# Performance work log

Hardware: AMD Instinct MI355X
Metric: run time of the kernel (lower is better)

Reference implementation:

```python
import jax, jax.numpy as jnp
import numpy as np

H = W = 56; WS = 7; SHIFT = 3; NH = 6; DIM = 192; DEPTH = 2
HD = DIM // NH; NW = (H // WS) * (W // WS); N = WS * WS; SCALE = HD ** -0.5

# relative position index (constant, as in WindowAttention.__init__)
_c = np.stack(np.meshgrid(np.arange(WS), np.arange(WS), indexing='ij')).reshape(2, -1)
_r = (_c[:, :, None] - _c[:, None, :]).transpose(1, 2, 0)
_r[..., 0] += WS - 1; _r[..., 1] += WS - 1; _r[..., 0] *= 2 * WS - 1
RPI = jnp.asarray(_r.sum(-1).reshape(-1))  # (N*N,)

def _build_mask():
    # shifted-window attention mask (constant, built in SwinTransformerBlock.__init__)
    img = np.zeros((H, W))
    sl = (slice(0, -WS), slice(-WS, -SHIFT), slice(-SHIFT, None))
    cnt = 0
    for hs in sl:
        for ws_ in sl:
            img[hs, ws_] = cnt; cnt += 1
    mw = img.reshape(H // WS, WS, W // WS, WS).transpose(0, 2, 1, 3).reshape(-1, N)
    am = mw[:, None, :] - mw[:, :, None]  # (nW, N, N)
    return jnp.asarray(np.where(am != 0, -100.0, 0.0).astype(np.float32))

MASK = _build_mask()

def _ln(x, g, b):
    m = jnp.mean(x, -1, keepdims=True)
    v = jnp.mean((x - m) ** 2, -1, keepdims=True)
    return (x - m) * jax.lax.rsqrt(v + 1e-5) * g + b

def setup_inputs() -> dict:
    key = jax.random.key(0)
    ks = jax.random.split(key, 8)
    B = 64; s = 0.02
    return {
        'x': jax.random.normal(ks[0], (B, H * W, DIM), jnp.float32),
        'norm1_g': jnp.ones((DEPTH, DIM), jnp.float32),
        'norm1_b': jnp.zeros((DEPTH, DIM), jnp.float32),
        'qkv_w': jax.random.normal(ks[1], (DEPTH, DIM, 3 * DIM), jnp.float32) * s,
        'qkv_b': jnp.zeros((DEPTH, 3 * DIM), jnp.float32),
        'rpb': jax.random.normal(ks[2], (DEPTH, (2 * WS - 1) ** 2, NH), jnp.float32) * s,
        'proj_w': jax.random.normal(ks[3], (DEPTH, DIM, DIM), jnp.float32) * s,
        'proj_b': jnp.zeros((DEPTH, DIM), jnp.float32),
        'norm2_g': jnp.ones((DEPTH, DIM), jnp.float32),
        'norm2_b': jnp.zeros((DEPTH, DIM), jnp.float32),
        'fc1_w': jax.random.normal(ks[4], (DEPTH, DIM, 4 * DIM), jnp.float32) * s,
        'fc1_b': jnp.zeros((DEPTH, 4 * DIM), jnp.float32),
        'fc2_w': jax.random.normal(ks[5], (DEPTH, 4 * DIM, DIM), jnp.float32) * s,
        'fc2_b': jnp.zeros((DEPTH, DIM), jnp.float32),
    }

def reference(x, norm1_g, norm1_b, qkv_w, qkv_b, rpb, proj_w, proj_b,
              norm2_g, norm2_b, fc1_w, fc1_b, fc2_w, fc2_b):
    B = x.shape[0]
    for i in range(DEPTH):
        shift = 0 if i % 2 == 0 else WS // 2
        # --- windowed MHSA branch ---
        h = _ln(x, norm1_g[i], norm1_b[i]).reshape(B, H, W, DIM)
        if shift:
            h = jnp.roll(h, (-shift, -shift), (1, 2))
        # window partition -> (B*nW, N, C)
        w = h.reshape(B, H // WS, WS, W // WS, WS, DIM)
        w = w.transpose(0, 1, 3, 2, 4, 5).reshape(B * NW, N, DIM)
        qkv = (w @ qkv_w[i] + qkv_b[i]).reshape(B * NW, N, 3, NH, HD)
        qkv = qkv.transpose(2, 0, 3, 1, 4)  # (3, Bw, NH, N, HD)
        q, k, v = qkv[0] * SCALE, qkv[1], qkv[2]
        attn = jnp.einsum('bhnd,bhmd->bhnm', q, k)  # (Bw, NH, N, N)
        bias = rpb[i][RPI].reshape(N, N, NH).transpose(2, 0, 1)
        attn = attn + bias[None]
        if shift:
            attn = attn.reshape(B, NW, NH, N, N) + MASK[None, :, None]
            attn = attn.reshape(B * NW, NH, N, N)
        attn = jax.nn.softmax(attn, axis=-1)
        o = jnp.einsum('bhnm,bhmd->bhnd', attn, v)
        o = o.transpose(0, 2, 1, 3).reshape(B * NW, N, DIM)
        o = o @ proj_w[i] + proj_b[i]
        # window reverse
        h = o.reshape(B, H // WS, W // WS, WS, WS, DIM)
        h = h.transpose(0, 1, 3, 2, 4, 5).reshape(B, H, W, DIM)
        if shift:
            h = jnp.roll(h, (shift, shift), (1, 2))
        x = x + h.reshape(B, H * W, DIM)
        # --- MLP branch ---
        m = _ln(x, norm2_g[i], norm2_b[i])
        m = jax.nn.gelu(m @ fc1_w[i] + fc1_b[i], approximate=False)
        x = x + (m @ fc2_w[i] + fc2_b[i])
    return x
```

## Files before the change

### kernel.cpp

```cpp
#include <hip/hip_runtime.h>
#include <stdint.h>

#define MROWS  200704
#define SCALE_ 0.17677669529663687f

typedef __attribute__((ext_vector_type(8))) short bf16x8;
typedef __attribute__((ext_vector_type(4))) float f32x4;
union V8 { uint4 u; unsigned short s[8]; };

__device__ __forceinline__ float bf2f(unsigned short u) {
  union { unsigned int i; float f; } c; c.i = ((unsigned int)u) << 16; return c.f;
}
__device__ __forceinline__ unsigned short f2bf(float f) {
  union { float f; unsigned int i; } c; c.f = f;
  unsigned int lsb = (c.i >> 16) & 1;
  return (unsigned short)((c.i + 0x7fffu + lsb) >> 16);
}

typedef __attribute__((address_space(1))) const void gas_t;
typedef __attribute__((address_space(3))) void las_t;
__device__ __forceinline__ void gload16(const void* g, void* l) {
  __builtin_amdgcn_global_load_lds((gas_t*)g, (las_t*)l, 16, 0, 0);
}

__device__ __forceinline__ bf16x8 ard(const unsigned short* As, int row, int k) {
  return *reinterpret_cast<const bf16x8*>(As + row * 192 + (((k >> 3) ^ (row & 7)) << 3));
}
__device__ __forceinline__ void awr(unsigned short* As, int row, int c, unsigned short v) {
  As[row * 192 + (((c >> 3) ^ (row & 7)) << 3) + (c & 7)] = v;
}
template<int RS>
__device__ __forceinline__ void stage_a(const unsigned short* __restrict__ src,
                                        unsigned short* As, int wv, int lane, int colofs) {
  #pragma unroll
  for (int i = 0; i < 12; ++i) {
    int g = wv * 768 + i * 64 + lane;
    int row = g / 24, c = g - row * 24;
    int sc = c ^ (row & 7);
    gload16(src + (size_t)row * RS + colofs + sc * 8, As + (wv * 768 + i * 64) * 8);
  }
}
__device__ __forceinline__ void ln_row(const float* __restrict__ xr,
    const float* __restrict__ g, const float* __restrict__ b,
    unsigned short* As, int row, int lane) {
  float v0 = xr[lane], v1 = xr[lane + 64], v2 = xr[lane + 128];
  float s  = v0 + v1 + v2;
  float s2 = v0*v0 + v1*v1 + v2*v2;
  #pragma unroll
  for (int m = 32; m >= 1; m >>= 1) { s += __shfl_xor(s, m); s2 += __shfl_xor(s2, m); }
  float mean = s * (1.0f/192.0f);
  float var  = s2 * (1.0f/192.0f) - mean*mean;
  float inv  = rsqrtf(var + 1e-5f);
  awr(As, row, lane,       f2bf((v0-mean)*inv*g[lane]      + b[lane]));
  awr(As, row, lane+64,    f2bf((v1-mean)*inv*g[lane+64]   + b[lane+64]));
  awr(As, row, lane+128,   f2bf((v2-mean)*inv*g[lane+128]  + b[lane+128]));
}
__device__ __forceinline__ void panel_mm(const bf16x8 (&afr)[6][4],
    const unsigned short* __restrict__ Wp, int kq, f32x4 (&acc)[4][2]) {
  bf16x8 bfr[6][2];
  #pragma unroll
  for (int ks = 0; ks < 6; ++ks) {
    bfr[ks][0] = *reinterpret_cast<const bf16x8*>(Wp + ks*32 + kq);
    bfr[ks][1] = *reinterpret_cast<const bf16x8*>(Wp + 16*192 + ks*32 + kq);
  }
  #pragma unroll
  for (int ks = 0; ks < 6; ++ks)
    #pragma unroll
    for (int mi = 0; mi < 4; ++mi) {
      acc[mi][0] = __builtin_amdgcn_mfma_f32_16x16x32_bf16(afr[ks][mi], bfr[ks][0], acc[mi][0], 0, 0, 0);
      acc[mi][1] = __builtin_amdgcn_mfma_f32_16x16x32_bf16(afr[ks][mi], bfr[ks][1], acc[mi][1], 0, 0, 0);
    }
}

__global__ __launch_bounds__(256) void wt_k(const float* __restrict__ W,
    unsigned short* __restrict__ Wt, int K, int N)
{
  int idx = blockIdx.x * 256 + threadIdx.x;
  if (idx < K * N) {
    int k = idx / N, n = idx - k * N;
    Wt[(size_t)n * K + k] = f2bf(W[idx]);
  }
}

__global__ __launch_bounds__(256, 2) void qkv_k(const float* __restrict__ X,
    const float* __restrict__ g, const float* __restrict__ b,
    const unsigned short* __restrict__ Wt, const float* __restrict__ bias,
    unsigned short* __restrict__ C, int shift)
{
  __shared__ unsigned short As[128 * 192];
  const int tid = threadIdx.x, lane = tid & 63, wv = tid >> 6;
  const int row0 = blockIdx.x * 128;
  #pragma unroll 2
  for (int r = 0; r < 32; ++r) {
    int row = wv * 32 + r, wr = row0 + row;
    int win = wr / 49, n = wr - win * 49;
    int bi = win >> 6, w64 = win & 63, wh = w64 >> 3, ww = w64 & 7;
    int ti = n / 7, tj = n - ti * 7;
    int gh = wh*7 + ti + shift; if (gh >= 56) gh -= 56;
    int gw = ww*7 + tj + shift; if (gw >= 56) gw -= 56;
    ln_row(X + ((size_t)bi*3136 + gh*56 + gw)*192, g, b, As, row, lane);
  }
  __syncthreads();
  const int wm = wv >> 1, wn = wv & 1, fr = lane & 15, kq = (lane >> 4) * 8;
  bf16x8 afr[6][4];
  #pragma unroll
  for (int ks = 0; ks < 6; ++ks)
    #pragma unroll
    for (int mi = 0; mi < 4; ++mi)
      afr[ks][mi] = ard(As, wm*64 + mi*16 + fr, ks*32 + kq);
  const int lcol = lane & 15, lr4 = (lane >> 4) * 4;
  #pragma unroll 2
  for (int p = 0; p < 9; ++p) {
    f32x4 acc[4][2] = {};
    panel_mm(afr, Wt + (size_t)(p*64 + wn*32 + fr) * 192, kq, acc);
    #pragma unroll
    for (int mi = 0; mi < 4; ++mi)
    #pragma unroll
    for (int ni = 0; ni < 2; ++ni)
    #pragma unroll
    for (int i = 0; i < 4; ++i) {
      int gr = row0 + wm*64 + mi*16 + lr4 + i;
      int gc = p*64 + wn*32 + ni*16 + lcol;
      C[(size_t)gr * 576 + gc] = f2bf(acc[mi][ni][i] + bias[gc]);
    }
  }
}

__global__ __launch_bounds__(256, 2) void proj_k(const unsigned short* __restrict__ A,
    const unsigned short* __restrict__ Wt, const float* __restrict__ bias,
    const float* __restrict__ Xres, float* __restrict__ Xdst, int shift)
{
  __shared__ unsigned short As[128 * 192];
  const int tid = threadIdx.x, lane = tid & 63, wv = tid >> 6;
  const int row0 = blockIdx.x * 128;
  stage_a<192>(A + (size_t)row0 * 192, As, wv, lane, 0);
  __syncthreads();
  const int wm = wv >> 1, wn = wv & 1, fr = lane & 15, kq = (lane >> 4) * 8;
  bf16x8 afr[6][4];
  #pragma unroll
  for (int ks = 0; ks < 6; ++ks)
    #pragma unroll
    for (int mi = 0; mi < 4; ++mi)
      afr[ks][mi] = ard(As, wm*64 + mi*16 + fr, ks*32 + kq);
  const int lcol = lane & 15, lr4 = (lane >> 4) * 4;
  int rbase[16];
  #pragma unroll
  for (int mi = 0; mi < 4; ++mi)
  #pragma unroll
  for (int i = 0; i < 4; ++i) {
    int gr = row0 + wm*64 + mi*16 + lr4 + i;
    int win = gr / 49, n = gr - win * 49;
    int bi = win >> 6, w64 = win & 63, wh = w64 >> 3, ww = w64 & 7;
    int ti = n / 7, tj = n - ti * 7;
    int gh = wh*7 + ti + shift; if (gh >= 56) gh -= 56;
    int gw = ww*7 + tj + shift; if (gw >= 56) gw -= 56;
    rbase[mi*4 + i] = (bi*3136 + gh*56 + gw) * 192;
  }
  #pragma unroll
  for (int p = 0; p < 3; ++p) {
    f32x4 acc[4][2] = {};
    panel_mm(afr, Wt + (size_t)(p*64 + wn*32 + fr) * 192, kq, acc);
    #pragma unroll
    for (int mi = 0; mi < 4; ++mi)
    #pragma unroll
    for (int ni = 0; ni < 2; ++ni)
    #pragma unroll
    for (int i = 0; i < 4; ++i) {
      int gc = p*64 + wn*32 + ni*16 + lcol;
      size_t idx = (size_t)rbase[mi*4 + i] + gc;
      Xdst[idx] = Xres[idx] + acc[mi][ni][i] + bias[gc];
    }
  }
}

__global__ __launch_bounds__(256, 2) void fc1_k(const float* __restrict__ X,
    const float* __restrict__ g, const float* __restrict__ b,
    const unsigned short* __restrict__ Wt, const float* __restrict__ bias,
    unsigned short* __restrict__ H)
{
  __shared__ unsigned short As[128 * 192];
  const int tid = threadIdx.x, lane = tid & 63, wv = tid >> 6;
  const int row0 = blockIdx.x * 128;
  #pragma unroll 2
  for (int r = 0; r < 32; ++r) {
    int row = wv * 32 + r;
    ln_row(X + (size_t)(row0 + row) * 192, g, b, As, row, lane);
  }
  __syncthreads();
  const int wm = wv >> 1, wn = wv & 1, fr = lane & 15, kq = (lane >> 4) * 8;
  bf16x8 afr[6][4];
  #pragma unroll
  for (int ks = 0; ks < 6; ++ks)
    #pragma unroll
    for (int mi = 0; mi < 4; ++mi)
      afr[ks][mi] = ard(As, wm*64 + mi*16 + fr, ks*32 + kq);
  const int lcol = lane & 15, lr4 = (lane >> 4) * 4;
  #pragma unroll 2
  for (int p = 0; p < 12; ++p) {
    f32x4 acc[4][2] = {};
    panel_mm(afr, Wt + (size_t)(p*64 + wn*32 + fr) * 192, kq, acc);
    #pragma unroll
    for (int mi = 0; mi < 4; ++mi)
    #pragma unroll
    for (int ni = 0; ni < 2; ++ni)
    #pragma unroll
    for (int i = 0; i < 4; ++i) {
      int gr = row0 + wm*64 + mi*16 + lr4 + i;
      int gc = p*64 + wn*32 + ni*16 + lcol;
      float v = acc[mi][ni][i] + bias[gc];
      float gv = 0.5f * v * (1.0f + erff(v * 0.70710678118654752f));
      H[(size_t)gr * 768 + gc] = f2bf(gv);
    }
  }
}

__global__ __launch_bounds__(256, 2) void fc2_k(const unsigned short* __restrict__ H,
    const unsigned short* __restrict__ Wt,
    const float* __restrict__ bias, const float* __restrict__ Xres,
    float* __restrict__ Y)
{
  __shared__ unsigned short As[128 * 192];
  const int tid = threadIdx.x, lane = tid & 63, wv = tid >> 6;
  const int row0 = blockIdx.x * 128;
  const int wm = wv >> 1, wn = wv & 1, fr = lane & 15, kq = (lane >> 4) * 8;
  f32x4 acc[3][4][2] = {};
  for (int q = 0; q < 4; ++q) {
    if (q) __syncthreads();
    stage_a<768>(H + (size_t)row0 * 768, As, wv, lane, q * 192);
    __syncthreads();
    #pragma unroll
    for (int ks = 0; ks < 6; ++ks) {
      bf16x8 afr[4];
      #pragma unroll
      for (int mi = 0; mi < 4; ++mi)
        afr[mi] = ard(As, wm*64 + mi*16 + fr, ks*32 + kq);
      #pragma unroll
      for (int p = 0; p < 3; ++p) {
        const unsigned short* wp = Wt + (size_t)(p*64 + wn*32 + fr) * 768 + q*192 + ks*32 + kq;
        bf16x8 b0 = *reinterpret_cast<const bf16x8*>(wp);
        bf16x8 b1 = *reinterpret_cast<const bf16x8*>(wp + 16*768);
        #pragma unroll
        for (int mi = 0; mi < 4; ++mi) {
          acc[p][mi][0] = __builtin_amdgcn_mfma_f32_16x16x32_bf16(afr[mi], b0, acc[p][mi][0], 0, 0, 0);
          acc[p][mi][1] = __builtin_amdgcn_mfma_f32_16x16x32_bf16(afr[mi], b1, acc[p][mi][1], 0, 0, 0);
        }
      }
    }
  }
  const int lcol = lane & 15, lr4 = (lane >> 4) * 4;
  #pragma unroll
  for (int p = 0; p < 3; ++p)
  #pragma unroll
  for (int mi = 0; mi < 4; ++mi)
  #pragma unroll
  for (int ni = 0; ni < 2; ++ni)
  #pragma unroll
  for (int i = 0; i < 4; ++i) {
    int grow = row0 + wm*64 + mi*16 + lr4 + i;
    int gc = p*64 + wn*32 + ni*16 + lcol;
    float v = acc[p][mi][ni][i] + bias[gc];
    size_t idx = (size_t)grow * 192 + gc;
    Y[idx] = Xres[idx] + v;
  }
}

template<bool SHIFTED>
__global__ __launch_bounds__(64) void attn_k(
    const unsigned short* __restrict__ qkv,
    const float* __restrict__ rpb,
    unsigned short* __restrict__ out)
{
  __shared__ float kv[2][49][32];
  int blk = blockIdx.x;
  int win = blk / 6, h = blk - win * 6;
  int lane = threadIdx.x;
  const unsigned short* base = qkv + (size_t)win * 49 * 576;
  for (int idx = lane; idx < 196; idx += 64) {
    int n = idx >> 2, sg = (idx & 3) * 8;
    V8 kk, vv;
    kk.u = *reinterpret_cast<const uint4*>(base + n*576 + 192 + h*32 + sg);
    vv.u = *reinterpret_cast<const uint4*>(base + n*576 + 384 + h*32 + sg);
    #pragma unroll
    for (int j = 0; j < 8; ++j) { kv[0][n][sg+j] = bf2f(kk.s[j]); kv[1][n][sg+j] = bf2f(vv.s[j]); }
  }
  __syncthreads();
  if (lane < 49) {
    float q[32];
    const unsigned short* qr = base + (size_t)lane * 576 + h * 32;
    #pragma unroll
    for (int sg = 0; sg < 4; ++sg) {
      V8 qq; qq.u = *reinterpret_cast<const uint4*>(qr + sg*8);
      #pragma unroll
      for (int j = 0; j < 8; ++j) q[sg*8+j] = bf2f(qq.s[j]) * SCALE_;
    }
    int ti = lane / 7, tj = lane - ti * 7;
    int wi = win & 63, wh = wi >> 3, ww = wi & 7;
    int rid = 0;
    if (SHIFTED) {
      int hh = wh*7 + ti, wg = ww*7 + tj;
      rid = (hh < 49 ? 0 : (hh < 53 ? 1 : 2)) * 3 + (wg < 49 ? 0 : (wg < 53 ? 1 : 2));
    }
    float s[49];
    float mx = -1e30f;
    #pragma unroll
    for (int m = 0; m < 49; ++m) {
      float a = 0.f;
      #pragma unroll
      for (int d4 = 0; d4 < 8; ++d4) {
        float4 kf = *reinterpret_cast<const float4*>(&kv[0][m][d4*4]);
        a += q[d4*4+0]*kf.x + q[d4*4+1]*kf.y + q[d4*4+2]*kf.z + q[d4*4+3]*kf.w;
      }
      int mi = m / 7, mj = m - mi * 7;
      a += rpb[((ti - mi + 6) * 13 + (tj - mj + 6)) * 6 + h];
      if (SHIFTED) {
        int hh = wh*7 + mi, wg = ww*7 + mj;
        int rid2 = (hh < 49 ? 0 : (hh < 53 ? 1 : 2)) * 3 + (wg < 49 ? 0 : (wg < 53 ? 1 : 2));
        if (rid2 != rid) a -= 100.f;
      }
      s[m] = a;
      mx = fmaxf(mx, a);
    }
    float sum = 0.f;
    #pragma unroll
    for (int m = 0; m < 49; ++m) { float e = __expf(s[m] - mx); s[m] = e; sum += e; }
    float rs = 1.f / sum;
    float o[32];
    #pragma unroll
    for (int d = 0; d < 32; ++d) o[d] = 0.f;
    #pragma unroll
    for (int m = 0; m < 49; ++m) {
      float p = s[m] * rs;
      #pragma unroll
      for (int d4 = 0; d4 < 8; ++d4) {
        float4 vf = *reinterpret_cast<const float4*>(&kv[1][m][d4*4]);
        o[d4*4+0] += p*vf.x; o[d4*4+1] += p*vf.y; o[d4*4+2] += p*vf.z; o[d4*4+3] += p*vf.w;
      }
    }
    unsigned short* orow = out + ((size_t)win * 49 + lane) * 192 + h * 32;
    #pragma unroll
    for (int sg = 0; sg < 4; ++sg) {
      V8 pk;
      #pragma unroll
      for (int j = 0; j < 8; ++j) pk.s[j] = f2bf(o[sg*8+j]);
      *reinterpret_cast<uint4*>(orow + sg*8) = pk.u;
    }
  }
}

extern "C" void kernel_launch(void* const* d_in, const int* in_sizes, int n_in,
                              void* d_out, int out_size, void* d_ws, size_t ws_size,
                              hipStream_t stream) {
  const float* x    = (const float*)d_in[0];
  const float* n1g  = (const float*)d_in[1];
  const float* n1b  = (const float*)d_in[2];
  const float* qkvw = (const float*)d_in[3];
  const float* qkvb = (const float*)d_in[4];
  const float* rpb  = (const float*)d_in[5];
  const float* pw   = (const float*)d_in[6];
  const float* pb   = (const float*)d_in[7];
  const float* n2g  = (const float*)d_in[8];
  const float* n2b  = (const float*)d_in[9];
  const float* f1w  = (const float*)d_in[10];
  const float* f1b  = (const float*)d_in[11];
  const float* f2w  = (const float*)d_in[12];
  const float* f2b  = (const float*)d_in[13];
  float* out = (float*)d_out;

  const size_t XBYTES = (size_t)MROWS * 192 * 4;
  const size_t QBYTES = (size_t)MROWS * 576 * 2;
  const size_t ABYTES = (size_t)MROWS * 192 * 2;
  char* ws = (char*)d_ws;
  float* x1 = (float*)ws;
  unsigned short* Bbuf = (unsigned short*)(ws + XBYTES);
  unsigned short* Abuf = (unsigned short*)(ws + XBYTES + QBYTES);
  unsigned short* Hbuf = Bbuf;
  unsigned short* WT   = (unsigned short*)(ws + XBYTES + QBYTES + ABYTES);
  const size_t WQ = 110592, WP = 36864, W1 = 147456, W2 = 147456;
  const size_t WD = WQ + WP + W1 + W2;

  for (int d = 0; d < 2; ++d) {
    unsigned short* wt = WT + d * WD;
    wt_k<<<(int)((WQ + 255)/256), 256, 0, stream>>>(qkvw + (size_t)d*WQ, wt,                 192, 576);
    wt_k<<<(int)((WP + 255)/256), 256, 0, stream>>>(pw   + (size_t)d*WP, wt + WQ,            192, 192);
    wt_k<<<(int)((W1 + 255)/256), 256, 0, stream>>>(f1w  + (size_t)d*W1, wt + WQ + WP,       192, 768);
    wt_k<<<(int)((W2 + 255)/256), 256, 0, stream>>>(f2w  + (size_t)d*W2, wt + WQ + WP + W1,  768, 192);
  }

  const int GB = MROWS / 128;

  for (int i = 0; i < 2; ++i) {
    int shift = i ? 3 : 0;
    const float* xin = i ? (const float*)x1 : x;
    float* xfin = i ? out : x1;
    const unsigned short* wt = WT + i * WD;
    qkv_k<<<GB, 256, 0, stream>>>(xin, n1g + i*192, n1b + i*192, wt, qkvb + i*576, Bbuf, shift);
    if (shift) attn_k<true ><<<4096*6, 64, 0, stream>>>(Bbuf, rpb + i*169*6, Abuf);
    else       attn_k<false><<<4096*6, 64, 0, stream>>>(Bbuf, rpb + i*169*6, Abuf);
    proj_k<<<GB, 256, 0, stream>>>(Abuf, wt + WQ, pb + i*192, xin, x1, shift);
    fc1_k<<<GB, 256, 0, stream>>>(x1, n2g + i*192, n2b + i*192, wt + WQ + WP, f1b + i*768, Hbuf);
    fc2_k<<<GB, 256, 0, stream>>>(Hbuf, wt + WQ + WP + W1, f2b + i*192, x1, xfin);
  }
}
```

Measured before the change: 2.072 ms.

## Fuse fc1+GELU+fc2 into one MLP kernel and vectorize GEMM epilogues

Replaces the separate fc1 and fc2 kernels with a single mlp_k that keeps the 64x768 hidden activation chunked in shared memory, so the bf16 hidden tensor never goes to global memory. Exact erf GELU is replaced by a tanh-form approximation computed with exp and rcp. The qkv and proj MFMAs swap operand order so each lane holds four consecutive columns, which allows packed bf16 and float4 epilogue stores. Risks are GELU approximation error, lower MFMA reuse per block with 64-row tiles, and W1/W2 being re-read from global per block.

Result: slower. 2.309 ms (+11.4%).

```diff
diff --git a/kernel.cpp b/kernel.cpp
--- a/kernel.cpp
+++ b/kernel.cpp
@@ -15,6 +15,19 @@
   union { float f; unsigned int i; } c; c.f = f;
   unsigned int lsb = (c.i >> 16) & 1;
   return (unsigned short)((c.i + 0x7fffu + lsb) >> 16);
+}
+__device__ __forceinline__ uint2 pack4(float a, float b, float c, float d) {
+  uint2 r;
+  r.x = (unsigned)f2bf(a) | ((unsigned)f2bf(b) << 16);
+  r.y = (unsigned)f2bf(c) | ((unsigned)f2bf(d) << 16);
+  return r;
+}
+__device__ __forceinline__ float gelu_f(float x) {
+  float x2 = x * x;
+  float arg = x * fmaf(0.07135481f, x2, 1.59576912f);
+  float e = __expf(arg);
+  float r = __builtin_amdgcn_rcpf(1.0f + e);
+  return fmaf(-x, r, x);
 }
 
 typedef __attribute__((address_space(1))) const void gas_t;
@@ -55,7 +68,7 @@
   awr(As, row, lane+64,    f2bf((v1-mean)*inv*g[lane+64]   + b[lane+64]));
   awr(As, row, lane+128,   f2bf((v2-mean)*inv*g[lane+128]  + b[lane+128]));
 }
-__device__ __forceinline__ void panel_mm(const bf16x8 (&afr)[6][4],
+__device__ __forceinline__ void panel_mmS(const bf16x8 (&afr)[6][4],
     const unsigned short* __restrict__ Wp, int kq, f32x4 (&acc)[4][2]) {
   bf16x8 bfr[6][2];
   #pragma unroll
@@ -67,8 +80,8 @@
   for (int ks = 0; ks < 6; ++ks)
     #pragma unroll
     for (int mi = 0; mi < 4; ++mi) {
-      acc[mi][0] = __builtin_amdgcn_mfma_f32_16x16x32_bf16(afr[ks][mi], bfr[ks][0], acc[mi][0], 0, 0, 0);
-      acc[mi][1] = __builtin_amdgcn_mfma_f32_16x16x32_bf16(afr[ks][mi], bfr[ks][1], acc[mi][1], 0, 0, 0);
+      acc[mi][0] = __builtin_amdgcn_mfma_f32_16x16x32_bf16(bfr[ks][0], afr[ks][mi], acc[mi][0], 0, 0, 0);
+      acc[mi][1] = __builtin_amdgcn_mfma_f32_16x16x32_bf16(bfr[ks][1], afr[ks][mi], acc[mi][1], 0, 0, 0);
     }
 }
 
@@ -101,27 +114,27 @@
     ln_row(X + ((size_t)bi*3136 + gh*56 + gw)*192, g, b, As, row, lane);
   }
   __syncthreads();
-  const int wm = wv >> 1, wn = wv & 1, fr = lane & 15, kq = (lane >> 4) * 8;
+  const int wm = wv >> 1, wn = wv & 1, l15 = lane & 15, kq = (lane >> 4) * 8, qd = lane >> 4;
   bf16x8 afr[6][4];
   #pragma unroll
   for (int ks = 0; ks < 6; ++ks)
     #pragma unroll
     for (int mi = 0; mi < 4; ++mi)
-      afr[ks][mi] = ard(As, wm*64 + mi*16 + fr, ks*32 + kq);
-  const int lcol = lane & 15, lr4 = (lane >> 4) * 4;
+      afr[ks][mi] = ard(As, wm*64 + mi*16 + l15, ks*32 + kq);
   #pragma unroll 2
   for (int p = 0; p < 9; ++p) {
     f32x4 acc[4][2] = {};
-    panel_mm(afr, Wt + (size_t)(p*64 + wn*32 + fr) * 192, kq, acc);
+    panel_mmS(afr, Wt + (size_t)(p*64 + wn*32 + l15) * 192, kq, acc);
     #pragma unroll
     for (int mi = 0; mi < 4; ++mi)
     #pragma unroll
-    for (int ni = 0; ni < 2; ++ni)
-    #pragma unroll
-    for (int i = 0; i < 4; ++i) {
-      int gr = row0 + wm*64 + mi*16 + lr4 + i;
-      int gc = p*64 + wn*32 + ni*16 + lcol;
-      C[(size_t)gr * 576 + gc] = f2bf(acc[mi][ni][i] + bias[gc]);
+    for (int ni = 0; ni < 2; ++ni) {
+      int row = row0 + wm*64 + mi*16 + l15;
+      int col = p*64 + wn*32 + ni*16 + qd*4;
+      float4 bv = *reinterpret_cast<const float4*>(bias + col);
+      uint2 pk = pack4(acc[mi][ni][0]+bv.x, acc[mi][ni][1]+bv.y,
+                       acc[mi][ni][2]+bv.z, acc[mi][ni][3]+bv.w);
+      *reinterpret_cast<uint2*>(C + (size_t)row * 576 + col) = pk;
     }
   }
 }
@@ -135,132 +148,139 @@
   const int row0 = blockIdx.x * 128;
   stage_a<192>(A + (size_t)row0 * 192, As, wv, lane, 0);
   __syncthreads();
-  const int wm = wv >> 1, wn = wv & 1, fr = lane & 15, kq = (lane >> 4) * 8;
+  const int wm = wv >> 1, wn = wv & 1, l15 = lane & 15, kq = (lane >> 4) * 8, qd = lane >> 4;
   bf16x8 afr[6][4];
   #pragma unroll
   for (int ks = 0; ks < 6; ++ks)
     #pragma unroll
     for (int mi = 0; mi < 4; ++mi)
-      afr[ks][mi] = ard(As, wm*64 + mi*16 + fr, ks*32 + kq);
-  const int lcol = lane & 15, lr4 = (lane >> 4) * 4;
-  int rbase[16];
-  #pragma unroll
-  for (int mi = 0; mi < 4; ++mi)
-  #pragma unroll
-  for (int i = 0; i < 4; ++i) {
-    int gr = row0 + wm*64 + mi*16 + lr4 + i;
+      afr[ks][mi] = ard(As, wm*64 + mi*16 + l15, ks*32 + kq);
+  int rbase[4];
+  #pragma unroll
+  for (int mi = 0; mi < 4; ++mi) {
+    int gr = row0 + wm*64 + mi*16 + l15;
     int win = gr / 49, n = gr - win * 49;
     int bi = win >> 6, w64 = win & 63, wh = w64 >> 3, ww = w64 & 7;
     int ti = n / 7, tj = n - ti * 7;
     int gh = wh*7 + ti + shift; if (gh >= 56) gh -= 56;
     int gw = ww*7 + tj + shift; if (gw >= 56) gw -= 56;
-    rbase[mi*4 + i] = (bi*3136 + gh*56 + gw) * 192;
+    rbase[mi] = (bi*3136 + gh*56 + gw) * 192;
   }
   #pragma unroll
   for (int p = 0; p < 3; ++p) {
     f32x4 acc[4][2] = {};
-    panel_mm(afr, Wt + (size_t)(p*64 + wn*32 + fr) * 192, kq, acc);
+    panel_mmS(afr, Wt + (size_t)(p*64 + wn*32 + l15) * 192, kq, acc);
     #pragma unroll
     for (int mi = 0; mi < 4; ++mi)
     #pragma unroll
-    for (int ni = 0; ni < 2; ++ni)
-    #pragma unroll
-    for (int i = 0; i < 4; ++i) {
-      int gc = p*64 + wn*32 + ni*16 + lcol;
-      size_t idx = (size_t)rbase[mi*4 + i] + gc;
-      Xdst[idx] = Xres[idx] + acc[mi][ni][i] + bias[gc];
-    }
-  }
-}
-
-__global__ __launch_bounds__(256, 2) void fc1_k(const float* __restrict__ X,
+    for (int ni = 0; ni < 2; ++ni) {
+      int col = p*64 + wn*32 + ni*16 + qd*4;
+      float4 bv = *reinterpret_cast<const float4*>(bias + col);
+      size_t idx = (size_t)rbase[mi] + col;
+      float4 xr = *reinterpret_cast<const float4*>(Xres + idx);
+      float4 o;
+      o.x = xr.x + acc[mi][ni][0] + bv.x; o.y = xr.y + acc[mi][ni][1] + bv.y;
+      o.z = xr.z + acc[mi][ni][2] + bv.z; o.w = xr.w + acc[mi][ni][3] + bv.w;
+      *reinterpret_cast<float4*>(Xdst + idx) = o;
+    }
+  }
+}
+
+__global__ __launch_bounds__(256, 2) void mlp_k(
+    const float* __restrict__ X,
     const float* __restrict__ g, const float* __restrict__ b,
-    const unsigned short* __restrict__ Wt, const float* __restrict__ bias,
-    unsigned short* __restrict__ H)
-{
-  __shared__ unsigned short As[128 * 192];
-  const int tid = threadIdx.x, lane = tid & 63, wv = tid >> 6;
-  const int row0 = blockIdx.x * 128;
-  #pragma unroll 2
-  for (int r = 0; r < 32; ++r) {
-    int row = wv * 32 + r;
-    ln_row(X + (size_t)(row0 + row) * 192, g, b, As, row, lane);
-  }
-  __syncthreads();
-  const int wm = wv >> 1, wn = wv & 1, fr = lane & 15, kq = (lane >> 4) * 8;
-  bf16x8 afr[6][4];
-  #pragma unroll
-  for (int ks = 0; ks < 6; ++ks)
-    #pragma unroll
-    for (int mi = 0; mi < 4; ++mi)
-      afr[ks][mi] = ard(As, wm*64 + mi*16 + fr, ks*32 + kq);
-  const int lcol = lane & 15, lr4 = (lane >> 4) * 4;
-  #pragma unroll 2
-  for (int p = 0; p < 12; ++p) {
-    f32x4 acc[4][2] = {};
-    panel_mm(afr, Wt + (size_t)(p*64 + wn*32 + fr) * 192, kq, acc);
-    #pragma unroll
-    for (int mi = 0; mi < 4; ++mi)
-    #pragma unroll
-    for (int ni = 0; ni < 2; ++ni)
-    #pragma unroll
-    for (int i = 0; i < 4; ++i) {
-      int gr = row0 + wm*64 + mi*16 + lr4 + i;
-      int gc = p*64 + wn*32 + ni*16 + lcol;
-      float v = acc[mi][ni][i] + bias[gc];
-      float gv = 0.5f * v * (1.0f + erff(v * 0.70710678118654752f));
-      H[(size_t)gr * 768 + gc] = f2bf(gv);
-    }
-  }
-}
-
-__global__ __launch_bounds__(256, 2) void fc2_k(const unsigned short* __restrict__ H,
-    const unsigned short* __restrict__ Wt,
-    const float* __restrict__ bias, const float* __restrict__ Xres,
+    const unsigned short* __restrict__ W1t,
+    const float* __restrict__ b1,
+    const unsigned short* __restrict__ W2t,
+    const float* __restrict__ b2,
     float* __restrict__ Y)
 {
-  __shared__ unsigned short As[128 * 192];
+  __shared__ unsigned short Hs[64][200];
+  const int row0 = blockIdx.x * 64;
   const int tid = threadIdx.x, lane = tid & 63, wv = tid >> 6;
-  const int row0 = blockIdx.x * 128;
-  const int wm = wv >> 1, wn = wv & 1, fr = lane & 15, kq = (lane >> 4) * 8;
-  f32x4 acc[3][4][2] = {};
+  const int l15 = lane & 15, qd = lane >> 4, kq = qd * 8;
+  const int wm = wv >> 1, wn = wv & 1;
+  #pragma unroll 2
+  for (int r = 0; r < 16; ++r) {
+    int row = wv * 16 + r;
+    const float* xr = X + (size_t)(row0 + row) * 192;
+    float v0 = xr[lane], v1 = xr[lane + 64], v2 = xr[lane + 128];
+    float s  = v0 + v1 + v2;
+    float s2 = v0*v0 + v1*v1 + v2*v2;
+    #pragma unroll
+    for (int m = 32; m >= 1; m >>= 1) { s += __shfl_xor(s, m); s2 += __shfl_xor(s2, m); }
+    float mean = s * (1.0f/192.0f);
+    float var  = s2 * (1.0f/192.0f) - mean*mean;
+    float inv  = rsqrtf(var + 1e-5f);
+    Hs[row][lane]     = f2bf((v0-mean)*inv*g[lane]      + b[lane]);
+    Hs[row][lane+64]  = f2bf((v1-mean)*inv*g[lane+64]   + b[lane+64]);
+    Hs[row][lane+128] = f2bf((v2-mean)*inv*g[lane+128]  + b[lane+128]);
+  }
+  __syncthreads();
+  bf16x8 afr[6][2];
+  #pragma unroll
+  for (int ks = 0; ks < 6; ++ks)
+    #pragma unroll
+    for (int mt = 0; mt < 2; ++mt)
+      afr[ks][mt] = *reinterpret_cast<const bf16x8*>(&Hs[wm*32 + mt*16 + l15][ks*32 + kq]);
+  f32x4 acc2[6][2] = {};
+  #pragma unroll 1
   for (int q = 0; q < 4; ++q) {
-    if (q) __syncthreads();
-    stage_a<768>(H + (size_t)row0 * 768, As, wv, lane, q * 192);
+    f32x4 acc1[6][2] = {};
+    #pragma unroll
+    for (int ks = 0; ks < 6; ++ks) {
+      bf16x8 w1f[6];
+      #pragma unroll
+      for (int ht = 0; ht < 6; ++ht)
+        w1f[ht] = *reinterpret_cast<const bf16x8*>(
+            &W1t[(size_t)(q*192 + wn*96 + ht*16 + l15) * 192 + ks*32 + kq]);
+      #pragma unroll
+      for (int ht = 0; ht < 6; ++ht)
+        #pragma unroll
+        for (int mt = 0; mt < 2; ++mt)
+          acc1[ht][mt] = __builtin_amdgcn_mfma_f32_16x16x32_bf16(w1f[ht], afr[ks][mt], acc1[ht][mt], 0, 0, 0);
+    }
     __syncthreads();
     #pragma unroll
+    for (int ht = 0; ht < 6; ++ht) {
+      float4 bv = *reinterpret_cast<const float4*>(b1 + q*192 + wn*96 + ht*16 + qd*4);
+      #pragma unroll
+      for (int mt = 0; mt < 2; ++mt) {
+        uint2 pk = pack4(gelu_f(acc1[ht][mt][0]+bv.x), gelu_f(acc1[ht][mt][1]+bv.y),
+                         gelu_f(acc1[ht][mt][2]+bv.z), gelu_f(acc1[ht][mt][3]+bv.w));
+        *reinterpret_cast<uint2*>(&Hs[wm*32 + mt*16 + l15][wn*96 + ht*16 + qd*4]) = pk;
+      }
+    }
+    __syncthreads();
+    #pragma unroll
     for (int ks = 0; ks < 6; ++ks) {
-      bf16x8 afr[4];
-      #pragma unroll
-      for (int mi = 0; mi < 4; ++mi)
-        afr[mi] = ard(As, wm*64 + mi*16 + fr, ks*32 + kq);
-      #pragma unroll
-      for (int p = 0; p < 3; ++p) {
-        const unsigned short* wp = Wt + (size_t)(p*64 + wn*32 + fr) * 768 + q*192 + ks*32 + kq;
-        bf16x8 b0 = *reinterpret_cast<const bf16x8*>(wp);
-        bf16x8 b1 = *reinterpret_cast<const bf16x8*>(wp + 16*768);
+      bf16x8 hbf[2];
+      #pragma unroll
+      for (int mt = 0; mt < 2; ++mt)
+        hbf[mt] = *reinterpret_cast<const bf16x8*>(&Hs[wm*32 + mt*16 + l15][ks*32 + kq]);
+      #pragma unroll
+      for (int ct = 0; ct < 6; ++ct) {
+        bf16x8 w2f = *reinterpret_cast<const bf16x8*>(
+            &W2t[(size_t)(wn*96 + ct*16 + l15) * 768 + q*192 + ks*32 + kq]);
         #pragma unroll
-        for (int mi = 0; mi < 4; ++mi) {
-          acc[p][mi][0] = __builtin_amdgcn_mfma_f32_16x16x32_bf16(afr[mi], b0, acc[p][mi][0], 0, 0, 0);
-          acc[p][mi][1] = __builtin_amdgcn_mfma_f32_16x16x32_bf16(afr[mi], b1, acc[p][mi][1], 0, 0, 0);
-        }
+        for (int mt = 0; mt < 2; ++mt)
+          acc2[ct][mt] = __builtin_amdgcn_mfma_f32_16x16x32_bf16(w2f, hbf[mt], acc2[ct][mt], 0, 0, 0);
       }
     }
   }
-  const int lcol = lane & 15, lr4 = (lane >> 4) * 4;
-  #pragma unroll
-  for (int p = 0; p < 3; ++p)
-  #pragma unroll
-  for (int mi = 0; mi < 4; ++mi)
-  #pragma unroll
-  for (int ni = 0; ni < 2; ++ni)
-  #pragma unroll
-  for (int i = 0; i < 4; ++i) {
-    int grow = row0 + wm*64 + mi*16 + lr4 + i;
-    int gc = p*64 + wn*32 + ni*16 + lcol;
-    float v = acc[p][mi][ni][i] + bias[gc];
-    size_t idx = (size_t)grow * 192 + gc;
-    Y[idx] = Xres[idx] + v;
+  #pragma unroll
+  for (int ct = 0; ct < 6; ++ct) {
+    int col = wn*96 + ct*16 + qd*4;
+    float4 bv = *reinterpret_cast<const float4*>(b2 + col);
+    #pragma unroll
+    for (int mt = 0; mt < 2; ++mt) {
+      size_t idx = (size_t)(row0 + wm*32 + mt*16 + l15) * 192 + col;
+      float4 xr = *reinterpret_cast<const float4*>(X + idx);
+      float4 o;
+      o.x = xr.x + acc2[ct][mt][0] + bv.x; o.y = xr.y + acc2[ct][mt][1] + bv.y;
+      o.z = xr.z + acc2[ct][mt][2] + bv.z; o.w = xr.w + acc2[ct][mt][3] + bv.w;
+      *reinterpret_cast<float4*>(Y + idx) = o;
+    }
   }
 }
 
@@ -373,7 +393,6 @@
   float* x1 = (float*)ws;
   unsigned short* Bbuf = (unsigned short*)(ws + XBYTES);
   unsigned short* Abuf = (unsigned short*)(ws + XBYTES + QBYTES);
-  unsigned short* Hbuf = Bbuf;
   unsigned short* WT   = (unsigned short*)(ws + XBYTES + QBYTES + ABYTES);
   const size_t WQ = 110592, WP = 36864, W1 = 147456, W2 = 147456;
   const size_t WD = WQ + WP + W1 + W2;
@@ -397,7 +416,8 @@
     if (shift) attn_k<true ><<<4096*6, 64, 0, stream>>>(Bbuf, rpb + i*169*6, Abuf);
     else       attn_k<false><<<4096*6, 64, 0, stream>>>(Bbuf, rpb + i*169*6, Abuf);
     proj_k<<<GB, 256, 0, stream>>>(Abuf, wt + WQ, pb + i*192, xin, x1, shift);
-    fc1_k<<<GB, 256, 0, stream>>>(x1, n2g + i*192, n2b + i*192, wt + WQ + WP, f1b + i*768, Hbuf);
-    fc2_k<<<GB, 256, 0, stream>>>(Hbuf, wt + WQ + WP + W1, f2b + i*192, x1, xfin);
-  }
-}
+    mlp_k<<<MROWS/64, 256, 0, stream>>>(x1, n2g + i*192, n2b + i*192,
+                                        wt + WQ + WP, f1b + i*768,
+                                        wt + WQ + WP + W1, f2b + i*192, xfin);
+  }
+}
```
